# Performance work log

Measured on AMD Instinct MI355X. Metric: run time of the kernel, lower is better.

## Reference

```python
import jax, jax.numpy as jnp
import numpy as np

B, T, I, H, O, L = 128, 512, 64, 256, 2, 2


def _gru_layer(x_seq, w_ih, w_hh, b_ih, b_hh):
    # x_seq: [B, T, in], w_ih: [3H, in], w_hh: [3H, H], biases: [3H]
    # PyTorch gate order: r, z, n
    xg = jnp.einsum('bti,gi->btg', x_seq, w_ih) + b_ih  # [B, T, 3H]
    h0 = jnp.zeros((x_seq.shape[0], w_hh.shape[1]), x_seq.dtype)

    def step(h, xg_t):
        hg = h @ w_hh.T + b_hh  # [B, 3H]
        xr, xz, xn = jnp.split(xg_t, 3, axis=-1)
        hr, hz, hn = jnp.split(hg, 3, axis=-1)
        r = jax.nn.sigmoid(xr + hr)
        z = jax.nn.sigmoid(xz + hz)
        n = jnp.tanh(xn + r * hn)
        h_new = (1.0 - z) * n + z * h
        return h_new, h_new

    _, hs = jax.lax.scan(step, h0, jnp.swapaxes(xg, 0, 1))  # [T, B, H]
    return jnp.swapaxes(hs, 0, 1)  # [B, T, H]


def setup_inputs() -> dict:
    key = jax.random.key(0)
    ks = jax.random.split(key, 12)
    s_ih0 = 1.0 / np.sqrt(H)
    inp = {
        'x': jax.random.normal(ks[0], (B, T, I), jnp.float32),
        'w_ih0': jax.random.uniform(ks[1], (3 * H, I), jnp.float32, -s_ih0, s_ih0),
        'w_hh0': jax.random.uniform(ks[2], (3 * H, H), jnp.float32, -s_ih0, s_ih0),
        'b_ih0': jax.random.uniform(ks[3], (3 * H,), jnp.float32, -s_ih0, s_ih0),
        'b_hh0': jax.random.uniform(ks[4], (3 * H,), jnp.float32, -s_ih0, s_ih0),
        'w_ih1': jax.random.uniform(ks[5], (3 * H, H), jnp.float32, -s_ih0, s_ih0),
        'w_hh1': jax.random.uniform(ks[6], (3 * H, H), jnp.float32, -s_ih0, s_ih0),
        'b_ih1': jax.random.uniform(ks[7], (3 * H,), jnp.float32, -s_ih0, s_ih0),
        'b_hh1': jax.random.uniform(ks[8], (3 * H,), jnp.float32, -s_ih0, s_ih0),
        'fc_w': jax.random.uniform(ks[9], (O, H), jnp.float32, -s_ih0, s_ih0),
        'fc_b': jax.random.uniform(ks[10], (O,), jnp.float32, -s_ih0, s_ih0),
    }
    return inp


def reference(x, w_ih0, w_hh0, b_ih0, b_hh0, w_ih1, w_hh1, b_ih1, b_hh1, fc_w, fc_b):
    h1 = _gru_layer(x, w_ih0, w_hh0, b_ih0, b_hh0)   # [B, T, H]
    h2 = _gru_layer(h1, w_ih1, w_hh1, b_ih1, b_hh1)  # [B, T, H]
    last = jax.nn.relu(h2[:, -1])                     # [B, H]
    return last @ fc_w.T + fc_b                       # [B, O]
```

## Files before the change

kernel.cpp:

```cpp
#include <hip/hip_runtime.h>


namespace {
constexpr int kB = 128, kT = 512, kI = 64, kH = 256;
constexpr int kBH = kB * kH;

constexpr int NG = 8, GW = 32, RPG = 16, NWG = NG * GW;
constexpr int NT = 512;

constexpr int P64 = 68, P256 = 260;

constexpr int O_W0IH = 0;
constexpr int O_W0HH = O_W0IH + 24 * P64;
constexpr int O_W1IH = O_W0HH + 24 * P256;
constexpr int O_W1HH = O_W1IH + 24 * P256;
constexpr int O_HS0  = O_W1HH + 24 * P256;
constexpr int O_HS1  = O_HS0 + RPG * P256;
constexpr int O_XS   = O_HS1 + RPG * P256;
constexpr int O_PB   = O_XS + RPG * P64;
constexpr int LDSF   = O_PB + 2 * 128 * 3;

constexpr int kFlagStride = 16;
}

__device__ __forceinline__ float sigf(float v) { return 1.0f / (1.0f + expf(-v)); }
__device__ __forceinline__ float dot4(const float4 a, const float4 b) {
  return a.x * b.x + a.y * b.y + a.z * b.z + a.w * b.w;
}
#define F4(p) (*(const float4*)(p))

__global__ __launch_bounds__(NT, 2) void gru_persistent(
    const float* __restrict__ x,
    const float* __restrict__ wih0, const float* __restrict__ whh0,
    const float* __restrict__ bih0, const float* __restrict__ bhh0,
    const float* __restrict__ wih1, const float* __restrict__ whh1,
    const float* __restrict__ bih1, const float* __restrict__ bhh1,
    const float* __restrict__ fcw, const float* __restrict__ fcb,
    float* __restrict__ h0buf, float* __restrict__ h1buf,
    unsigned* flags, float* __restrict__ out)
{
  __shared__ float lds[LDSF];

  const int bid = blockIdx.x;
  const int g   = bid >> 5;
  const int wg  = bid & (GW - 1);
  const int tid = threadIdx.x;
  const int j0  = wg * 8;
  const int r0  = g * RPG;

  for (int i = tid; i < 24 * 16; i += NT) {
    const int r = i >> 4, c = (i & 15) * 4, gg = r >> 3, u2 = r & 7;
    *(float4*)(lds + O_W0IH + r * P64 + c) =
        F4(wih0 + (size_t)(gg * kH + j0 + u2) * kI + c);
  }
  for (int i = tid; i < 24 * 64; i += NT) {
    const int r = i >> 6, c = (i & 63) * 4, gg = r >> 3, u2 = r & 7;
    const size_t src = (size_t)(gg * kH + j0 + u2) * kH + c;
    *(float4*)(lds + O_W0HH + r * P256 + c) = F4(whh0 + src);
    *(float4*)(lds + O_W1IH + r * P256 + c) = F4(wih1 + src);
    *(float4*)(lds + O_W1HH + r * P256 + c) = F4(whh1 + src);
  }

  const int lay = (tid >> 8) & 1;
  const int fam = (tid >> 7) & 1;
  const int t6  = tid & 63;
  const int row = ((tid >> 6) & 1) * 8 + (t6 >> 3);
  const int uu  = t6 & 7;
  const int t7  = row * 8 + uu;
  const int j   = j0 + uu;

  const float* bi = lay ? bih1 : bih0;
  const float* bh = lay ? bhh1 : bhh0;
  const float br_r = bi[j] + bh[j];
  const float br_z = bi[kH + j] + bh[kH + j];
  const float bn_i = bi[2 * kH + j];
  const float bn_h = bh[2 * kH + j];

  const float* ax  = lds + O_XS  + row * P64;
  const float* ah0 = lds + O_HS0 + row * P256;
  const float* ah1 = lds + O_HS1 + row * P256;
  const float* w0i_r = lds + O_W0IH + (0 * 8 + uu) * P64;
  const float* w0i_z = lds + O_W0IH + (1 * 8 + uu) * P64;
  const float* w0i_n = lds + O_W0IH + (2 * 8 + uu) * P64;
  const float* w0h_r = lds + O_W0HH + (0 * 8 + uu) * P256;
  const float* w0h_z = lds + O_W0HH + (1 * 8 + uu) * P256;
  const float* w0h_n = lds + O_W0HH + (2 * 8 + uu) * P256;
  const float* w1x_r = (fam == 0) ? lds + O_W1IH + (0 * 8 + uu) * P256
                                  : lds + O_W1HH + (0 * 8 + uu) * P256;
  const float* w1x_z = (fam == 0) ? lds + O_W1IH + (1 * 8 + uu) * P256
                                  : lds + O_W1HH + (1 * 8 + uu) * P256;
  const float* w1x_n = (fam == 0) ? lds + O_W1IH + (2 * 8 + uu) * P256
                                  : lds + O_W1HH + (2 * 8 + uu) * P256;
  const float* a1 = (fam == 0) ? ah0 : ah1;

  unsigned* myflag = flags + (unsigned)((g << 5) + (tid & 31)) * kFlagStride;

  __syncthreads();

  for (int s = 0; s <= kT; ++s) {
    {
      const float* h0p = h0buf + (size_t)((s + 1) & 1) * kBH;
      const float* h1p = h1buf + (size_t)(s & 1) * kBH;
      #pragma unroll
      for (int p = 0; p < 4; ++p) {
        const int i = tid + p * NT;
        const int r = i >> 7, c = i & 127;
        const unsigned long long v0 = __hip_atomic_load(
            (const unsigned long long*)(h0p + (size_t)(r0 + r) * kH) + c,
            __ATOMIC_RELAXED, __HIP_MEMORY_SCOPE_AGENT);
        const unsigned long long v1 = __hip_atomic_load(
            (const unsigned long long*)(h1p + (size_t)(r0 + r) * kH) + c,
            __ATOMIC_RELAXED, __HIP_MEMORY_SCOPE_AGENT);
        float2 f0, f1;
        __builtin_memcpy(&f0, &v0, 8);
        __builtin_memcpy(&f1, &v1, 8);
        *(float2*)(lds + O_HS0 + r * P256 + c * 2) = f0;
        *(float2*)(lds + O_HS1 + r * P256 + c * 2) = f1;
      }
      if (s < kT && tid < 256) {
        const int r = tid >> 4, c4 = (tid & 15) * 4;
        *(float4*)(lds + O_XS + r * P64 + c4) =
            F4(x + (size_t)(r0 + r) * kT * kI + (size_t)s * kI + c4);
      }
    }
    __syncthreads();

    float p0 = 0.f, p1 = 0.f, p2 = 0.f;
    if (lay == 0) {
      if (fam == 0) {
        #pragma unroll
        for (int c = 0; c < 16; ++c) {
          const float4 a = F4(ax + c * 4);
          p0 += dot4(a, F4(w0i_r + c * 4));
          p1 += dot4(a, F4(w0i_z + c * 4));
          p2 += dot4(a, F4(w0i_n + c * 4));
        }
        #pragma unroll 6
        for (int c = 0; c < 36; ++c) {
          const float4 a = F4(ah0 + c * 4);
          p0 += dot4(a, F4(w0h_r + c * 4));
          p1 += dot4(a, F4(w0h_z + c * 4));
        }
      } else {
        #pragma unroll 6
        for (int c = 0; c < 36; ++c)
          p2 += dot4(F4(ah0 + c * 4), F4(w0h_n + c * 4));
        #pragma unroll 7
        for (int c = 36; c < 64; ++c) {
          const float4 a = F4(ah0 + c * 4);
          p0 += dot4(a, F4(w0h_r + c * 4));
          p1 += dot4(a, F4(w0h_z + c * 4));
          p2 += dot4(a, F4(w0h_n + c * 4));
        }
      }
    } else {
      #pragma unroll 8
      for (int c = 0; c < 64; ++c) {
        const float4 a = F4(a1 + c * 4);
        p0 += dot4(a, F4(w1x_r + c * 4));
        p1 += dot4(a, F4(w1x_z + c * 4));
        p2 += dot4(a, F4(w1x_n + c * 4));
      }
    }
    if (fam == 0) {
      float* pb = lds + O_PB + (lay * 128 + t7) * 3;
      pb[0] = p0; pb[1] = p1; pb[2] = p2;
    }
    __syncthreads();

    const bool act = lay ? (s >= 1) : (s < kT);
    if (fam == 1 && act) {
      const float* pb = lds + O_PB + (lay * 128 + t7) * 3;
      const float rr = sigf(pb[0] + p0 + br_r);
      const float zz = sigf(pb[1] + p1 + br_z);
      const float nn = tanhf(pb[2] + bn_i + rr * (p2 + bn_h));
      const float hp = (lay ? ah1 : ah0)[j];
      const float hv = (1.f - zz) * nn + zz * hp;
      float* hout = lay ? (h1buf + (size_t)((s + 1) & 1) * kBH)
                        : (h0buf + (size_t)(s & 1) * kBH);
      __hip_atomic_store(hout + (size_t)(r0 + row) * kH + j, hv,
                         __ATOMIC_RELAXED, __HIP_MEMORY_SCOPE_AGENT);
    }
    __syncthreads();

    if (tid == 0) {
      __hip_atomic_store(flags + (unsigned)bid * kFlagStride,
                         (unsigned)(s + 1),
                         __ATOMIC_RELAXED, __HIP_MEMORY_SCOPE_AGENT);
    }
    while (__hip_atomic_load(myflag, __ATOMIC_RELAXED,
                             __HIP_MEMORY_SCOPE_AGENT) < (unsigned)(s + 1)) {
      __builtin_amdgcn_s_sleep(1);
    }
    asm volatile("" ::: "memory");
    __syncthreads();
  }

  if (wg == 0 && tid < 256) {
    const int rv = tid >> 4, o = (tid >> 3) & 1, ks = tid & 7;
    const float* hf = h1buf + (size_t)kBH + (size_t)(r0 + rv) * kH;
    const float* wfc = fcw + (size_t)o * kH;
    float acc = 0.f;
    #pragma unroll 8
    for (int k = ks * 32; k < ks * 32 + 32; ++k) {
      const float hv = __hip_atomic_load(hf + k, __ATOMIC_RELAXED,
                                         __HIP_MEMORY_SCOPE_AGENT);
      acc += fmaxf(hv, 0.f) * wfc[k];
    }
    acc += __shfl_xor(acc, 1);
    acc += __shfl_xor(acc, 2);
    acc += __shfl_xor(acc, 4);
    if (ks == 0) out[(r0 + rv) * 2 + o] = acc + fcb[o];
  }
}

extern "C" void kernel_launch(void* const* d_in, const int* in_sizes, int n_in,
                              void* d_out, int out_size, void* d_ws, size_t ws_size,
                              hipStream_t stream) {
  const float* x    = (const float*)d_in[0];
  const float* wih0 = (const float*)d_in[1];
  const float* whh0 = (const float*)d_in[2];
  const float* bih0 = (const float*)d_in[3];
  const float* bhh0 = (const float*)d_in[4];
  const float* wih1 = (const float*)d_in[5];
  const float* whh1 = (const float*)d_in[6];
  const float* bih1 = (const float*)d_in[7];
  const float* bhh1 = (const float*)d_in[8];
  const float* fcw  = (const float*)d_in[9];
  const float* fcb  = (const float*)d_in[10];

  float* h0buf = (float*)d_ws;
  float* h1buf = h0buf + 2 * kBH;
  unsigned* flags = (unsigned*)(h1buf + 2 * kBH);
  float* out = (float*)d_out;

  hipMemsetAsync(d_ws, 0,
                 (size_t)(4 * kBH) * sizeof(float) +
                 (size_t)NWG * kFlagStride * sizeof(unsigned), stream);

  gru_persistent<<<NWG, NT, 0, stream>>>(
      x, wih0, whh0, bih0, bhh0, wih1, whh1, bih1, bhh1,
      fcw, fcb, h0buf, h1buf, flags, out);
}
```

Before: 3.915 ms.

## Keep GRU weight slices in registers and split the K dimension across lanes

Each thread now holds its slice of the input and recurrent weights in registers instead of reading them from LDS every step. The reduction dimension is split across 8 lane groups, with partial sums combined by xor-shuffles. The LDS hidden-state buffer is re-laid out into k-segments, and a separate pass of 256 threads applies the gates. One trailing barrier per step is also dropped. The aim is to cut per-step LDS traffic and the length of the serial dot products in this latency-bound recurrence. In exchange it raises register pressure, which risks spills under the two-blocks-per-CU launch bound, and adds shuffle and LDS partial-sum traffic.

```diff
diff --git a/kernel.cpp b/kernel.cpp
--- a/kernel.cpp
+++ b/kernel.cpp
@@ -2,23 +2,17 @@
 
 
 namespace {
-constexpr int kB = 128, kT = 512, kI = 64, kH = 256;
-constexpr int kBH = kB * kH;
-
-constexpr int NG = 8, GW = 32, RPG = 16, NWG = NG * GW;
-constexpr int NT = 512;
-
-constexpr int P64 = 68, P256 = 260;
-
-constexpr int O_W0IH = 0;
-constexpr int O_W0HH = O_W0IH + 24 * P64;
-constexpr int O_W1IH = O_W0HH + 24 * P256;
-constexpr int O_W1HH = O_W1IH + 24 * P256;
-constexpr int O_HS0  = O_W1HH + 24 * P256;
-constexpr int O_HS1  = O_HS0 + RPG * P256;
-constexpr int O_XS   = O_HS1 + RPG * P256;
-constexpr int O_PB   = O_XS + RPG * P64;
-constexpr int LDSF   = O_PB + 2 * 128 * 3;
+constexpr int kB = 128, kT = 512, kI = 64, kH = 256, kBH = kB * kH;
+constexpr int NG = 8, GW = 32, RPG = 16, NWG = 256, NT = 512;
+
+constexpr int SRS = 36;
+constexpr int SKS = 16 * SRS + 4;
+constexpr int O_S0 = 0;
+constexpr int O_S1 = O_S0 + 8 * SKS;
+constexpr int O_X  = O_S1 + 8 * SKS;
+constexpr int O_PB = O_X + RPG * 68;
+constexpr int PBN  = 4 * 16 * 36;
+constexpr int LDSF = O_PB + PBN;
 
 constexpr int kFlagStride = 16;
 }
@@ -26,6 +20,12 @@
 __device__ __forceinline__ float sigf(float v) { return 1.0f / (1.0f + expf(-v)); }
 __device__ __forceinline__ float dot4(const float4 a, const float4 b) {
   return a.x * b.x + a.y * b.y + a.z * b.z + a.w * b.w;
+}
+__device__ __forceinline__ float red8(float v) {
+  v += __shfl_xor(v, 8);
+  v += __shfl_xor(v, 16);
+  v += __shfl_xor(v, 32);
+  return v;
 }
 #define F4(p) (*(const float4*)(p))
 
@@ -45,53 +45,56 @@
   const int g   = bid >> 5;
   const int wg  = bid & (GW - 1);
   const int tid = threadIdx.x;
+  const int r0  = g * RPG;
   const int j0  = wg * 8;
-  const int r0  = g * RPG;
-
-  for (int i = tid; i < 24 * 16; i += NT) {
-    const int r = i >> 4, c = (i & 15) * 4, gg = r >> 3, u2 = r & 7;
-    *(float4*)(lds + O_W0IH + r * P64 + c) =
-        F4(wih0 + (size_t)(gg * kH + j0 + u2) * kI + c);
-  }
-  for (int i = tid; i < 24 * 64; i += NT) {
-    const int r = i >> 6, c = (i & 63) * 4, gg = r >> 3, u2 = r & 7;
-    const size_t src = (size_t)(gg * kH + j0 + u2) * kH + c;
-    *(float4*)(lds + O_W0HH + r * P256 + c) = F4(whh0 + src);
-    *(float4*)(lds + O_W1IH + r * P256 + c) = F4(wih1 + src);
-    *(float4*)(lds + O_W1HH + r * P256 + c) = F4(whh1 + src);
-  }
-
-  const int lay = (tid >> 8) & 1;
-  const int fam = (tid >> 7) & 1;
-  const int t6  = tid & 63;
-  const int row = ((tid >> 6) & 1) * 8 + (t6 >> 3);
-  const int uu  = t6 & 7;
-  const int t7  = row * 8 + uu;
-  const int j   = j0 + uu;
-
-  const float* bi = lay ? bih1 : bih0;
-  const float* bh = lay ? bhh1 : bhh0;
-  const float br_r = bi[j] + bh[j];
-  const float br_z = bi[kH + j] + bh[kH + j];
-  const float bn_i = bi[2 * kH + j];
-  const float bn_h = bh[2 * kH + j];
-
-  const float* ax  = lds + O_XS  + row * P64;
-  const float* ah0 = lds + O_HS0 + row * P256;
-  const float* ah1 = lds + O_HS1 + row * P256;
-  const float* w0i_r = lds + O_W0IH + (0 * 8 + uu) * P64;
-  const float* w0i_z = lds + O_W0IH + (1 * 8 + uu) * P64;
-  const float* w0i_n = lds + O_W0IH + (2 * 8 + uu) * P64;
-  const float* w0h_r = lds + O_W0HH + (0 * 8 + uu) * P256;
-  const float* w0h_z = lds + O_W0HH + (1 * 8 + uu) * P256;
-  const float* w0h_n = lds + O_W0HH + (2 * 8 + uu) * P256;
-  const float* w1x_r = (fam == 0) ? lds + O_W1IH + (0 * 8 + uu) * P256
-                                  : lds + O_W1HH + (0 * 8 + uu) * P256;
-  const float* w1x_z = (fam == 0) ? lds + O_W1IH + (1 * 8 + uu) * P256
-                                  : lds + O_W1HH + (1 * 8 + uu) * P256;
-  const float* w1x_n = (fam == 0) ? lds + O_W1IH + (2 * 8 + uu) * P256
-                                  : lds + O_W1HH + (2 * 8 + uu) * P256;
-  const float* a1 = (fam == 0) ? ah0 : ah1;
+
+  const int wave = tid >> 6;
+  const int lane = tid & 63;
+  const int lay  = wave >> 2;
+  const int fam  = (wave >> 1) & 1;
+  const int rh   = wave & 1;
+  const int ju   = lane & 7;
+  const int ks   = lane >> 3;
+  const int jg   = j0 + ju;
+
+  for (int i = tid; i < PBN; i += NT) lds[O_PB + i] = 0.f;
+
+  float4 wr0[8], wr1[8], wr2[8];
+  if (lay == 0) {
+    if (fam == 0) {
+#define L0F0(wrg, gg) { \
+      const float* wi = wih0 + (size_t)((gg) * kH + jg) * kI + ks * 8;   \
+      const float* wh = whh0 + (size_t)((gg) * kH + jg) * kH + ks * 32;  \
+      wrg[0] = F4(wi); wrg[1] = F4(wi + 4);                              \
+      wrg[2] = F4(wh); wrg[3] = F4(wh + 4); wrg[4] = F4(wh + 8); }
+      L0F0(wr0, 0) L0F0(wr1, 1) L0F0(wr2, 2)
+    } else {
+#define L0F1(wrg, gg) { \
+      const float* wh = whh0 + (size_t)((gg) * kH + jg) * kH + ks * 32 + 12; \
+      wrg[0] = F4(wh); wrg[1] = F4(wh + 4); wrg[2] = F4(wh + 8);             \
+      wrg[3] = F4(wh + 12); wrg[4] = F4(wh + 16); }
+      L0F1(wr0, 0) L0F1(wr1, 1) L0F1(wr2, 2)
+    }
+  } else {
+    const float* ws = fam ? whh1 : wih1;
+#define L1W(wrg, gg) { \
+    const float* wp = ws + (size_t)((gg) * kH + jg) * kH + ks * 32;          \
+    wrg[0] = F4(wp);      wrg[1] = F4(wp + 4);  wrg[2] = F4(wp + 8);         \
+    wrg[3] = F4(wp + 12); wrg[4] = F4(wp + 16); wrg[5] = F4(wp + 20);        \
+    wrg[6] = F4(wp + 24); wrg[7] = F4(wp + 28); }
+    L1W(wr0, 0) L1W(wr1, 1) L1W(wr2, 2)
+  }
+
+  float fb_r = 0.f, fb_z = 0.f, fb_ni = 0.f, fb_nh = 0.f;
+  if (tid < 256) {
+    const int layf = tid >> 7, uf = tid & 7, jf = j0 + uf;
+    const float* bi = layf ? bih1 : bih0;
+    const float* bh = layf ? bhh1 : bhh0;
+    fb_r  = bi[jf] + bh[jf];
+    fb_z  = bi[kH + jf] + bh[kH + jf];
+    fb_ni = bi[2 * kH + jf];
+    fb_nh = bh[2 * kH + jf];
+  }
 
   unsigned* myflag = flags + (unsigned)((g << 5) + (tid & 31)) * kFlagStride;
 
@@ -103,83 +106,118 @@
       const float* h1p = h1buf + (size_t)(s & 1) * kBH;
       #pragma unroll
       for (int p = 0; p < 4; ++p) {
-        const int i = tid + p * NT;
-        const int r = i >> 7, c = i & 127;
+        const int i  = tid + p * NT;
+        const int ro = i >> 7, k2 = i & 127;
+        const int k  = k2 * 2, ksg = k >> 5, off = k & 31;
         const unsigned long long v0 = __hip_atomic_load(
-            (const unsigned long long*)(h0p + (size_t)(r0 + r) * kH) + c,
+            (const unsigned long long*)(h0p + (size_t)(r0 + ro) * kH) + k2,
             __ATOMIC_RELAXED, __HIP_MEMORY_SCOPE_AGENT);
         const unsigned long long v1 = __hip_atomic_load(
-            (const unsigned long long*)(h1p + (size_t)(r0 + r) * kH) + c,
+            (const unsigned long long*)(h1p + (size_t)(r0 + ro) * kH) + k2,
             __ATOMIC_RELAXED, __HIP_MEMORY_SCOPE_AGENT);
         float2 f0, f1;
         __builtin_memcpy(&f0, &v0, 8);
         __builtin_memcpy(&f1, &v1, 8);
-        *(float2*)(lds + O_HS0 + r * P256 + c * 2) = f0;
-        *(float2*)(lds + O_HS1 + r * P256 + c * 2) = f1;
+        *(float2*)(lds + O_S0 + ksg * SKS + ro * SRS + off) = f0;
+        *(float2*)(lds + O_S1 + ksg * SKS + ro * SRS + off) = f1;
       }
       if (s < kT && tid < 256) {
-        const int r = tid >> 4, c4 = (tid & 15) * 4;
-        *(float4*)(lds + O_XS + r * P64 + c4) =
-            F4(x + (size_t)(r0 + r) * kT * kI + (size_t)s * kI + c4);
+        const int ro = tid >> 4, c4 = (tid & 15) * 4;
+        *(float4*)(lds + O_X + ro * 68 + c4) =
+            F4(x + (size_t)(r0 + ro) * kT * kI + (size_t)s * kI + c4);
       }
     }
     __syncthreads();
 
-    float p0 = 0.f, p1 = 0.f, p2 = 0.f;
-    if (lay == 0) {
-      if (fam == 0) {
-        #pragma unroll
-        for (int c = 0; c < 16; ++c) {
-          const float4 a = F4(ax + c * 4);
-          p0 += dot4(a, F4(w0i_r + c * 4));
-          p1 += dot4(a, F4(w0i_z + c * 4));
-          p2 += dot4(a, F4(w0i_n + c * 4));
+    const bool wact = lay ? (s >= 1) : (s < kT);
+    if (wact) {
+      float prr[8], pzz[8], pni[8], pnh[8];
+      #pragma unroll
+      for (int r = 0; r < 8; ++r) {
+        const int ro = rh * 8 + r;
+        float pr = 0.f, pz = 0.f, pxi = 0.f, pxh = 0.f;
+        if (lay == 0) {
+          if (fam == 0) {
+            const float* ax = lds + O_X + ro * 68 + ks * 8;
+            const float4 x0 = F4(ax), x1 = F4(ax + 4);
+            pr  += dot4(x0, wr0[0]) + dot4(x1, wr0[1]);
+            pz  += dot4(x0, wr1[0]) + dot4(x1, wr1[1]);
+            pxi += dot4(x0, wr2[0]) + dot4(x1, wr2[1]);
+            const float* ah = lds + O_S0 + ks * SKS + ro * SRS;
+            #pragma unroll
+            for (int i = 0; i < 3; ++i) {
+              const float4 hv = F4(ah + i * 4);
+              pr  += dot4(hv, wr0[2 + i]);
+              pz  += dot4(hv, wr1[2 + i]);
+              pxh += dot4(hv, wr2[2 + i]);
+            }
+          } else {
+            const float* ah = lds + O_S0 + ks * SKS + ro * SRS + 12;
+            #pragma unroll
+            for (int i = 0; i < 5; ++i) {
+              const float4 hv = F4(ah + i * 4);
+              pr  += dot4(hv, wr0[i]);
+              pz  += dot4(hv, wr1[i]);
+              pxh += dot4(hv, wr2[i]);
+            }
+          }
+        } else {
+          const float* aa = lds + (fam ? O_S1 : O_S0) + ks * SKS + ro * SRS;
+          #pragma unroll
+          for (int i = 0; i < 8; ++i) {
+            const float4 av = F4(aa + i * 4);
+            pr += dot4(av, wr0[i]);
+            pz += dot4(av, wr1[i]);
+            if (fam) pxh += dot4(av, wr2[i]);
+            else     pxi += dot4(av, wr2[i]);
+          }
         }
-        #pragma unroll 6
-        for (int c = 0; c < 36; ++c) {
-          const float4 a = F4(ah0 + c * 4);
-          p0 += dot4(a, F4(w0h_r + c * 4));
-          p1 += dot4(a, F4(w0h_z + c * 4));
+        prr[r] = pr; pzz[r] = pz; pni[r] = pxi; pnh[r] = pxh;
+      }
+      #pragma unroll
+      for (int r = 0; r < 8; ++r) { prr[r] = red8(prr[r]); pzz[r] = red8(pzz[r]); }
+      if (lay == 0 && fam == 0) {
+        #pragma unroll
+        for (int r = 0; r < 8; ++r) { pni[r] = red8(pni[r]); pnh[r] = red8(pnh[r]); }
+      } else if (fam == 0) {
+        #pragma unroll
+        for (int r = 0; r < 8; ++r) pni[r] = red8(pni[r]);
+      } else {
+        #pragma unroll
+        for (int r = 0; r < 8; ++r) pnh[r] = red8(pnh[r]);
+      }
+      if (ks == 0) {
+        #pragma unroll
+        for (int r = 0; r < 8; ++r) {
+          float* pb = lds + O_PB + ((wave >> 1) * 16 + rh * 8 + r) * SRS + ju;
+          pb[0] = prr[r]; pb[8] = pzz[r];
+          if (lay == 0 && fam == 0) { pb[16] = pni[r]; pb[24] = pnh[r]; }
+          else if (fam == 0)          pb[16] = pni[r];
+          else                        pb[24] = pnh[r];
         }
-      } else {
-        #pragma unroll 6
-        for (int c = 0; c < 36; ++c)
-          p2 += dot4(F4(ah0 + c * 4), F4(w0h_n + c * 4));
-        #pragma unroll 7
-        for (int c = 36; c < 64; ++c) {
-          const float4 a = F4(ah0 + c * 4);
-          p0 += dot4(a, F4(w0h_r + c * 4));
-          p1 += dot4(a, F4(w0h_z + c * 4));
-          p2 += dot4(a, F4(w0h_n + c * 4));
-        }
-      }
-    } else {
-      #pragma unroll 8
-      for (int c = 0; c < 64; ++c) {
-        const float4 a = F4(a1 + c * 4);
-        p0 += dot4(a, F4(w1x_r + c * 4));
-        p1 += dot4(a, F4(w1x_z + c * 4));
-        p2 += dot4(a, F4(w1x_n + c * 4));
-      }
-    }
-    if (fam == 0) {
-      float* pb = lds + O_PB + (lay * 128 + t7) * 3;
-      pb[0] = p0; pb[1] = p1; pb[2] = p2;
+      }
     }
     __syncthreads();
 
-    const bool act = lay ? (s >= 1) : (s < kT);
-    if (fam == 1 && act) {
-      const float* pb = lds + O_PB + (lay * 128 + t7) * 3;
-      const float rr = sigf(pb[0] + p0 + br_r);
-      const float zz = sigf(pb[1] + p1 + br_z);
-      const float nn = tanhf(pb[2] + bn_i + rr * (p2 + bn_h));
-      const float hp = (lay ? ah1 : ah0)[j];
-      const float hv = (1.f - zz) * nn + zz * hp;
-      float* hout = lay ? (h1buf + (size_t)((s + 1) & 1) * kBH)
-                        : (h0buf + (size_t)(s & 1) * kBH);
-      __hip_atomic_store(hout + (size_t)(r0 + row) * kH + j, hv,
-                         __ATOMIC_RELAXED, __HIP_MEMORY_SCOPE_AGENT);
+    if (tid < 256) {
+      const int layf = tid >> 7;
+      const bool act = layf ? (s >= 1) : (s < kT);
+      if (act) {
+        const int rof = (tid >> 3) & 15, uf = tid & 7, jf = j0 + uf;
+        const float* p0 = lds + O_PB + ((layf * 2) * 16 + rof) * SRS + uf;
+        const float* p1 = p0 + 16 * SRS;
+        const float rr = sigf(p0[0] + p1[0] + fb_r);
+        const float zz = sigf(p0[8] + p1[8] + fb_z);
+        const float nn = tanhf(p0[16] + p1[16] + fb_ni +
+                               rr * (p0[24] + p1[24] + fb_nh));
+        const float hp = lds[(layf ? O_S1 : O_S0) +
+                             (jf >> 5) * SKS + rof * SRS + (jf & 31)];
+        const float hv = (1.f - zz) * nn + zz * hp;
+        float* hout = layf ? (h1buf + (size_t)((s + 1) & 1) * kBH)
+                           : (h0buf + (size_t)(s & 1) * kBH);
+        __hip_atomic_store(hout + (size_t)(r0 + rof) * kH + jf, hv,
+                           __ATOMIC_RELAXED, __HIP_MEMORY_SCOPE_AGENT);
+      }
     }
     __syncthreads();
 
@@ -193,16 +231,15 @@
       __builtin_amdgcn_s_sleep(1);
     }
     asm volatile("" ::: "memory");
-    __syncthreads();
   }
 
   if (wg == 0 && tid < 256) {
-    const int rv = tid >> 4, o = (tid >> 3) & 1, ks = tid & 7;
+    const int rv = tid >> 4, o = (tid >> 3) & 1, kseg = tid & 7;
     const float* hf = h1buf + (size_t)kBH + (size_t)(r0 + rv) * kH;
     const float* wfc = fcw + (size_t)o * kH;
     float acc = 0.f;
     #pragma unroll 8
-    for (int k = ks * 32; k < ks * 32 + 32; ++k) {
+    for (int k = kseg * 32; k < kseg * 32 + 32; ++k) {
       const float hv = __hip_atomic_load(hf + k, __ATOMIC_RELAXED,
                                          __HIP_MEMORY_SCOPE_AGENT);
       acc += fmaxf(hv, 0.f) * wfc[k];
@@ -210,7 +247,7 @@
     acc += __shfl_xor(acc, 1);
     acc += __shfl_xor(acc, 2);
     acc += __shfl_xor(acc, 4);
-    if (ks == 0) out[(r0 + rv) * 2 + o] = acc + fcb[o];
+    if (kseg == 0) out[(r0 + rv) * 2 + o] = acc + fcb[o];
   }
 }
 
```

After: 3.779 ms. -3.5%, faster.
